# Kernel optimization log

Hardware: AMD Instinct MI355X
Metric: run time of the kernel (lower is better)

Reference implementation:

```python
import jax, jax.numpy as jnp
import numpy as np


def setup_inputs() -> dict:
    key = jax.random.key(0)
    k1, k2 = jax.random.split(key)
    B, EMB, CODES, NUM_TOKENS = 16, 64, 16384, 1024
    x_in = jax.random.normal(k1, (B, EMB, CODES), dtype=jnp.float32)
    code_embedding = jax.random.uniform(k2, (NUM_TOKENS, EMB), dtype=jnp.float32)
    return {"x_in": x_in, "code_embedding": code_embedding}


def reference(x_in, code_embedding):
    # x_in: [B, emb, codes]; code_embedding: [num_tokens, emb]
    x_t = jnp.transpose(x_in, (0, 2, 1))  # [B, codes, emb]
    # squared euclidean distances (argmin is invariant to sqrt used by cdist)
    x2 = jnp.sum(x_t * x_t, axis=-1)                      # [B, codes]
    e2 = jnp.sum(code_embedding * code_embedding, axis=-1)  # [num_tokens]
    dots = jnp.einsum('bce,ke->bck', x_t, code_embedding)   # [B, codes, num_tokens]
    dist2 = x2[:, :, None] - 2.0 * dots + e2[None, None, :]
    indices = jnp.argmin(dist2, axis=2)                   # [B, codes]
    x_out = jnp.transpose(code_embedding[indices], (0, 2, 1))  # [B, emb, codes]
    return x_out, indices[:, :, None]  # indices keepdim like torch argmin(keepdim=True)
```

## Files before the change

kernel.cpp:

```cpp
#include <hip/hip_runtime.h>


#define BB 16
#define EMB 64
#define CODES 16384
#define NT 1024
#define NTILES 64
#define CHUNK 8
#define EPOCHS (NTILES / CHUNK)
#define QPB 256

typedef __attribute__((ext_vector_type(8))) short s16x8;
typedef __attribute__((ext_vector_type(4))) float f32x4;
typedef __attribute__((ext_vector_type(4))) int i32x4;
typedef unsigned int u32;

__device__ inline short bf16_hi(float f) { return (short)(__builtin_bit_cast(u32, f) >> 16); }
__device__ inline float hi_part(float f) { return __builtin_bit_cast(float, __builtin_bit_cast(u32, f) & 0xFFFF0000u); }
__device__ inline u32 umax_(u32 a, u32 b) { return a > b ? a : b; }

__device__ inline void async_copy16(const char* g, char* lds_base_uniform) {
  __builtin_amdgcn_global_load_lds(
      (const __attribute__((address_space(1))) unsigned int*)g,
      (__attribute__((address_space(3))) unsigned int*)(unsigned int)(unsigned long long)lds_base_uniform,
      16, 0, 0);
}

#define WSE_OFF   0
#define WSH_OFF   266240
#define WSH2_OFF  270336

__global__ __launch_bounds__(256) void vq_prep(const float* __restrict__ E,
                                               char* __restrict__ wsE,
                                               float* __restrict__ wsh,
                                               float* __restrict__ wsh2) {
  const int bid = blockIdx.x, tid = threadIdx.x;
  if (bid < 32) {
    const int gid = bid * 256 + tid;
    const int nt = gid >> 7, ks = (gid >> 6) & 1, lane = gid & 63;
    const int col = lane & 15, quad = lane >> 4;
    const int n = nt * 16 + col;
    const int k0 = ks * 32 + quad * 8;
    const float* ep = E + n * EMB + k0;
    s16x8 hv, lv;
    #pragma unroll
    for (int j = 0; j < 8; ++j) {
      float v = ep[j];
      float hf = hi_part(v);
      hv[j] = bf16_hi(v);
      lv[j] = bf16_hi(v - hf);
    }
    char* base = wsE + ((size_t)nt << 12) + ((size_t)ks << 10) + lane * 16;
    *(i32x4*)(base)        = __builtin_bit_cast(i32x4, hv);
    *(i32x4*)(base + 2048) = __builtin_bit_cast(i32x4, lv);
  } else {
    const int n = (bid - 32) * 256 + tid;
    if (n < NT) {
      const float4* ep = (const float4*)(E + n * EMB);
      float s = 0.f;
      #pragma unroll
      for (int g = 0; g < 16; ++g) { float4 v = ep[g]; s += v.x*v.x + v.y*v.y + v.z*v.z + v.w*v.w; }
      const float h = -0.5f * s;
      wsh[n] = h;
      wsh2[n] = 16384.f * (h + 128.f);
    }
  }
}

__global__ __launch_bounds__(512, 4) void vq_main(
    const float* __restrict__ x, const float* __restrict__ E,
    const char* __restrict__ wsE, const float* __restrict__ wsh,
    const float* __restrict__ wsh2,
    float* __restrict__ xout, float* __restrict__ iout) {
  __shared__ char smem[2 * CHUNK * 4096 + 4096];
  float* lh = (float*)(smem + 2 * CHUNK * 4096);
  const int tid = threadIdx.x;
  const int wave = tid >> 6, lane = tid & 63;
  const int col = lane & 15, quad = lane >> 4;
  const int b = blockIdx.y;
  const int c0 = blockIdx.x * QPB;
  const int cw = c0 + wave * 32;

  ((float2*)lh)[tid] = ((const float2*)wsh2)[tid];
  {
    const char* g = wsE + wave * 4096 + lane * 16;
    char* lb = smem + wave * 4096;
    async_copy16(g,        lb);
    async_copy16(g + 1024, lb + 1024);
    async_copy16(g + 2048, lb + 2048);
    async_copy16(g + 3072, lb + 3072);
  }

  s16x8 ah[2][2], al[2][2];
  #pragma unroll
  for (int mt = 0; mt < 2; ++mt) {
    #pragma unroll
    for (int ks = 0; ks < 2; ++ks) {
      s16x8 hv, lv;
      #pragma unroll
      for (int j = 0; j < 8; ++j) {
        const int e = ks * 32 + quad * 8 + j;
        float v = x[((size_t)b * EMB + e) * CODES + (size_t)(cw + mt * 16 + col)] * 16384.f;
        float hf = hi_part(v);
        hv[j] = bf16_hi(v);
        lv[j] = bf16_hi(v - hf);
      }
      ah[mt][ks] = hv;
      al[mt][ks] = lv;
    }
  }

  u32 k1[2][4], k2[2][4];
  #pragma unroll
  for (int mt = 0; mt < 2; ++mt)
    #pragma unroll
    for (int r = 0; r < 4; ++r) { k1[mt][r] = 0u; k2[mt][r] = 0u; }

  u32 inv = 1023u - (u32)col;

  __syncthreads();

  for (int c = 0; c < EPOCHS; ++c) {
    if (c < EPOCHS - 1) {
      const char* g = wsE + (size_t)(c + 1) * (CHUNK * 4096) + wave * 4096 + lane * 16;
      char* lb = smem + ((c + 1) & 1) * (CHUNK * 4096) + wave * 4096;
      async_copy16(g,        lb);
      async_copy16(g + 1024, lb + 1024);
      async_copy16(g + 2048, lb + 2048);
      async_copy16(g + 3072, lb + 3072);
    }

    const char* rb = smem + (c & 1) * (CHUNK * 4096) + lane * 16;
    i32x4 fb0 = *(const i32x4*)(rb);
    i32x4 fb1 = *(const i32x4*)(rb + 1024);
    i32x4 fb2 = *(const i32x4*)(rb + 2048);
    i32x4 fb3 = *(const i32x4*)(rb + 3072);
    float ch = lh[(c * CHUNK) * 16 + col];

    #pragma unroll
    for (int t = 0; t < CHUNK; ++t) {
      i32x4 nb0, nb1, nb2, nb3; float nch;
      if (t < CHUNK - 1) {
        const char* p = rb + (t + 1) * 4096;
        nb0 = *(const i32x4*)(p);
        nb1 = *(const i32x4*)(p + 1024);
        nb2 = *(const i32x4*)(p + 2048);
        nb3 = *(const i32x4*)(p + 3072);
        nch = lh[(c * CHUNK + t + 1) * 16 + col];
      }
      const s16x8 bh0 = __builtin_bit_cast(s16x8, fb0);
      const s16x8 bh1 = __builtin_bit_cast(s16x8, fb1);
      const s16x8 bl0 = __builtin_bit_cast(s16x8, fb2);
      const s16x8 bl1 = __builtin_bit_cast(s16x8, fb3);
      const f32x4 cq = (f32x4){ch, ch, ch, ch};
      const f32x4 zz = (f32x4){0.f, 0.f, 0.f, 0.f};

      #pragma unroll
      for (int mt = 0; mt < 2; ++mt) {
        f32x4 cA = __builtin_amdgcn_mfma_f32_16x16x32_bf16(ah[mt][0], bh0, cq, 0, 0, 0);
        f32x4 cB = __builtin_amdgcn_mfma_f32_16x16x32_bf16(al[mt][1], bh1, zz, 0, 0, 0);
        cA = __builtin_amdgcn_mfma_f32_16x16x32_bf16(ah[mt][1], bh1, cA, 0, 0, 0);
        cB = __builtin_amdgcn_mfma_f32_16x16x32_bf16(ah[mt][0], bl0, cB, 0, 0, 0);
        cA = __builtin_amdgcn_mfma_f32_16x16x32_bf16(al[mt][0], bh0, cA, 0, 0, 0);
        cB = __builtin_amdgcn_mfma_f32_16x16x32_bf16(ah[mt][1], bl1, cB, 0, 0, 0);
        const f32x4 a = cA + cB;

        #pragma unroll
        for (int r = 0; r < 4; ++r) {
          u32 q = (u32)a[r];
          u32 key = (q << 10) + inv;
          u32 k1o = k1[mt][r];
          asm("v_med3_u32 %0, %1, %2, %3"
              : "=v"(k2[mt][r]) : "v"(key), "v"(k1o), "v"(k2[mt][r]));
          k1[mt][r] = umax_(key, k1o);
        }
      }
      inv -= 16u;
      if (t < CHUNK - 1) { fb0 = nb0; fb1 = nb1; fb2 = nb2; fb3 = nb3; ch = nch; }
    }
    __syncthreads();
  }

  uint2* cand = (uint2*)smem;
  int* idxs = (int*)(smem + 2048);
  #pragma unroll
  for (int mt = 0; mt < 2; ++mt) {
    #pragma unroll
    for (int r = 0; r < 4; ++r) {
      u32 a1 = k1[mt][r], a2 = k2[mt][r];
      #pragma unroll
      for (int m = 1; m <= 8; m <<= 1) {
        u32 r1 = __shfl_xor(a1, m, 64);
        u32 r2 = __shfl_xor(a2, m, 64);
        u32 t = a1 < r1 ? a1 : r1;
        a1 = umax_(a1, r1);
        a2 = umax_(umax_(a2, r2), t);
      }
      if (col == r) cand[wave * 32 + mt * 16 + quad * 4 + r] = make_uint2(a1, a2);
    }
  }
  __syncthreads();

  {
    const int q = tid >> 1, which = tid & 1;
    const u32 K = which ? cand[q].y : cand[q].x;
    const int i = 1023 - (int)(K & 1023u);
    const float* xq = x + (size_t)b * EMB * CODES + (size_t)(c0 + q);
    const float4* ei = (const float4*)(E + i * EMB);
    float d0 = 0, d1 = 0, d2 = 0, d3 = 0;
    #pragma unroll
    for (int g = 0; g < 16; ++g) {
      float4 a = ei[g];
      d0 = fmaf(xq[(size_t)(4 * g + 0) * CODES], a.x, d0);
      d1 = fmaf(xq[(size_t)(4 * g + 1) * CODES], a.y, d1);
      d2 = fmaf(xq[(size_t)(4 * g + 2) * CODES], a.z, d2);
      d3 = fmaf(xq[(size_t)(4 * g + 3) * CODES], a.w, d3);
    }
    const float s = ((d0 + d1) + (d2 + d3)) + wsh[i];
    const float s_o = __shfl_xor(s, 1, 64);
    const int i_o = __shfl_xor(i, 1, 64);
    if (which == 0) {
      const bool take2 = (s_o > s) || (s_o == s && i_o < i);
      const int idx = take2 ? i_o : i;
      idxs[q] = idx;
      iout[(size_t)b * CODES + (size_t)(c0 + q)] = (float)idx;
    }
  }
  __syncthreads();

  {
    const int q = tid & (QPB - 1);
    const int eh = (tid >> 8) * 32;
    const int idx = idxs[q];
    const float* Er = E + idx * EMB + eh;
    float* xo = xout + ((size_t)b * EMB + eh) * CODES + (size_t)(c0 + q);
    #pragma unroll
    for (int e = 0; e < 32; ++e) xo[(size_t)e * CODES] = Er[e];
  }
}

extern "C" void kernel_launch(void* const* d_in, const int* in_sizes, int n_in,
                              void* d_out, int out_size, void* d_ws, size_t ws_size,
                              hipStream_t stream) {
  const float* x = (const float*)d_in[0];
  const float* E = (const float*)d_in[1];
  float* xout = (float*)d_out;
  float* iout = (float*)d_out + (size_t)BB * EMB * CODES;

  char* wsE  = (char*)d_ws + WSE_OFF;
  float* wsh  = (float*)((char*)d_ws + WSH_OFF);
  float* wsh2 = (float*)((char*)d_ws + WSH2_OFF);

  vq_prep<<<36, 256, 0, stream>>>(E, wsE, wsh, wsh2);
  vq_main<<<dim3(CODES / QPB, BB), 512, 0, stream>>>(x, E, wsE, wsh, wsh2, xout, iout);
}
```

Before: 208.5 us.

## Software-pipeline tile loop with inline-asm LDS reads and deferred top-2 update

Replaces the per-tile unrolled loop with hand-scheduled inline-asm ds_read_b128 loads that double-buffer tiles in registers, gated by explicit lgkmcnt waits and sched barriers. The MFMAs for both row tiles are interleaved into independent chains. The argmin top-2 key update for each tile is deferred until the next tile's MFMAs are issued, and a final update runs after the loop. The goal is to hide LDS latency and the MFMA dependency chains behind independent work. In exchange it adds register pressure from the extra live accumulators and takes scheduling control away from the compiler.

```diff
diff --git a/kernel.cpp b/kernel.cpp
--- a/kernel.cpp
+++ b/kernel.cpp
@@ -67,6 +67,64 @@
   }
 }
 
+#define DS_READ_TILE(d0, d1, d2, d3, base, T)                               \
+  asm volatile("ds_read_b128 %0, %4 offset:%c5\n\t"                         \
+               "ds_read_b128 %1, %4 offset:%c6\n\t"                         \
+               "ds_read_b128 %2, %4 offset:%c7\n\t"                         \
+               "ds_read_b128 %3, %4 offset:%c8"                             \
+               : "=v"(d0), "=v"(d1), "=v"(d2), "=v"(d3)                     \
+               : "v"(base), "i"((T) * 4096), "i"((T) * 4096 + 1024),        \
+                 "i"((T) * 4096 + 2048), "i"((T) * 4096 + 3072))
+
+#define WAIT_SB(N)                                                          \
+  do {                                                                      \
+    asm volatile("s_waitcnt lgkmcnt(" #N ")");                              \
+    __builtin_amdgcn_sched_barrier(0);                                      \
+  } while (0)
+
+#define MFMA16 __builtin_amdgcn_mfma_f32_16x16x32_bf16
+
+#define TILE_MATH(F0, F1, F2, F3, CH)                                       \
+  do {                                                                      \
+    const s16x8 bh0 = __builtin_bit_cast(s16x8, F0);                        \
+    const s16x8 bh1 = __builtin_bit_cast(s16x8, F1);                        \
+    const s16x8 bl0 = __builtin_bit_cast(s16x8, F2);                        \
+    const s16x8 bl1 = __builtin_bit_cast(s16x8, F3);                        \
+    const f32x4 cq = (f32x4){CH, CH, CH, CH};                               \
+    const f32x4 zz = (f32x4){0.f, 0.f, 0.f, 0.f};                           \
+    f32x4 cA0 = MFMA16(ah[0][0], bh0, cq, 0, 0, 0);                         \
+    f32x4 cB0 = MFMA16(al[0][1], bh1, zz, 0, 0, 0);                         \
+    f32x4 cA1 = MFMA16(ah[1][0], bh0, cq, 0, 0, 0);                         \
+    f32x4 cB1 = MFMA16(al[1][1], bh1, zz, 0, 0, 0);                         \
+    cA0 = MFMA16(ah[0][1], bh1, cA0, 0, 0, 0);                              \
+    cB0 = MFMA16(ah[0][0], bl0, cB0, 0, 0, 0);                              \
+    cA1 = MFMA16(ah[1][1], bh1, cA1, 0, 0, 0);                              \
+    cB1 = MFMA16(ah[1][0], bl0, cB1, 0, 0, 0);                              \
+    cA0 = MFMA16(al[0][0], bh0, cA0, 0, 0, 0);                              \
+    cB0 = MFMA16(ah[0][1], bl1, cB0, 0, 0, 0);                              \
+    cA1 = MFMA16(al[1][0], bh0, cA1, 0, 0, 0);                              \
+    cB1 = MFMA16(ah[1][1], bl1, cB1, 0, 0, 0);                              \
+    TOP2(aPrev0, 0);                                                        \
+    TOP2(aPrev1, 1);                                                        \
+    aPrev0 = cA0 + cB0;                                                     \
+    aPrev1 = cA1 + cB1;                                                     \
+    invPrev = invCur;                                                       \
+    invCur -= 16u;                                                          \
+  } while (0)
+
+#define TOP2(AV, MT)                                                        \
+  do {                                                                      \
+    _Pragma("unroll")                                                       \
+    for (int r = 0; r < 4; ++r) {                                           \
+      u32 q = (u32)AV[r];                        \
+      u32 key = (q << 10) + invPrev;                                        \
+      u32 k1o = k1[MT][r];                                                  \
+      asm("v_med3_u32 %0, %1, %2, %3"                                       \
+          : "=v"(k2[MT][r]) : "v"(key), "v"(k1o), "v"(k2[MT][r]));          \
+      k1[MT][r] = umax_(key, k1o);                                          \
+    }                                                                       \
+  } while (0)
+
 __global__ __launch_bounds__(512, 4) void vq_main(
     const float* __restrict__ x, const float* __restrict__ E,
     const char* __restrict__ wsE, const float* __restrict__ wsh,
@@ -116,7 +174,10 @@
     #pragma unroll
     for (int r = 0; r < 4; ++r) { k1[mt][r] = 0u; k2[mt][r] = 0u; }
 
-  u32 inv = 1023u - (u32)col;
+  f32x4 aPrev0 = (f32x4){0.f, 0.f, 0.f, 0.f};
+  f32x4 aPrev1 = (f32x4){0.f, 0.f, 0.f, 0.f};
+  u32 invCur = 1023u - (u32)col;
+  u32 invPrev = 0u;
 
   __syncthreads();
 
@@ -130,56 +191,60 @@
       async_copy16(g + 3072, lb + 3072);
     }
 
-    const char* rb = smem + (c & 1) * (CHUNK * 4096) + lane * 16;
-    i32x4 fb0 = *(const i32x4*)(rb);
-    i32x4 fb1 = *(const i32x4*)(rb + 1024);
-    i32x4 fb2 = *(const i32x4*)(rb + 2048);
-    i32x4 fb3 = *(const i32x4*)(rb + 3072);
-    float ch = lh[(c * CHUNK) * 16 + col];
-
-    #pragma unroll
-    for (int t = 0; t < CHUNK; ++t) {
-      i32x4 nb0, nb1, nb2, nb3; float nch;
-      if (t < CHUNK - 1) {
-        const char* p = rb + (t + 1) * 4096;
-        nb0 = *(const i32x4*)(p);
-        nb1 = *(const i32x4*)(p + 1024);
-        nb2 = *(const i32x4*)(p + 2048);
-        nb3 = *(const i32x4*)(p + 3072);
-        nch = lh[(c * CHUNK + t + 1) * 16 + col];
-      }
-      const s16x8 bh0 = __builtin_bit_cast(s16x8, fb0);
-      const s16x8 bh1 = __builtin_bit_cast(s16x8, fb1);
-      const s16x8 bl0 = __builtin_bit_cast(s16x8, fb2);
-      const s16x8 bl1 = __builtin_bit_cast(s16x8, fb3);
-      const f32x4 cq = (f32x4){ch, ch, ch, ch};
-      const f32x4 zz = (f32x4){0.f, 0.f, 0.f, 0.f};
-
-      #pragma unroll
-      for (int mt = 0; mt < 2; ++mt) {
-        f32x4 cA = __builtin_amdgcn_mfma_f32_16x16x32_bf16(ah[mt][0], bh0, cq, 0, 0, 0);
-        f32x4 cB = __builtin_amdgcn_mfma_f32_16x16x32_bf16(al[mt][1], bh1, zz, 0, 0, 0);
-        cA = __builtin_amdgcn_mfma_f32_16x16x32_bf16(ah[mt][1], bh1, cA, 0, 0, 0);
-        cB = __builtin_amdgcn_mfma_f32_16x16x32_bf16(ah[mt][0], bl0, cB, 0, 0, 0);
-        cA = __builtin_amdgcn_mfma_f32_16x16x32_bf16(al[mt][0], bh0, cA, 0, 0, 0);
-        cB = __builtin_amdgcn_mfma_f32_16x16x32_bf16(ah[mt][1], bl1, cB, 0, 0, 0);
-        const f32x4 a = cA + cB;
-
-        #pragma unroll
-        for (int r = 0; r < 4; ++r) {
-          u32 q = (u32)a[r];
-          u32 key = (q << 10) + inv;
-          u32 k1o = k1[mt][r];
-          asm("v_med3_u32 %0, %1, %2, %3"
-              : "=v"(k2[mt][r]) : "v"(key), "v"(k1o), "v"(k2[mt][r]));
-          k1[mt][r] = umax_(key, k1o);
-        }
-      }
-      inv -= 16u;
-      if (t < CHUNK - 1) { fb0 = nb0; fb1 = nb1; fb2 = nb2; fb3 = nb3; ch = nch; }
-    }
+    const float ch0 = lh[(c * CHUNK + 0) * 16 + col];
+    const float ch1 = lh[(c * CHUNK + 1) * 16 + col];
+    const float ch2 = lh[(c * CHUNK + 2) * 16 + col];
+    const float ch3 = lh[(c * CHUNK + 3) * 16 + col];
+    const float ch4 = lh[(c * CHUNK + 4) * 16 + col];
+    const float ch5 = lh[(c * CHUNK + 5) * 16 + col];
+    const float ch6 = lh[(c * CHUNK + 6) * 16 + col];
+    const float ch7 = lh[(c * CHUNK + 7) * 16 + col];
+    asm volatile("" :: "v"(ch0), "v"(ch1), "v"(ch2), "v"(ch3),
+                       "v"(ch4), "v"(ch5), "v"(ch6), "v"(ch7));
+
+    const unsigned base =
+        (unsigned)(unsigned long long)(smem) +
+        (unsigned)((c & 1) * (CHUNK * 4096)) + (unsigned)(lane * 16);
+
+    i32x4 tA0, tA1, tA2, tA3, tB0, tB1, tB2, tB3;
+    DS_READ_TILE(tA0, tA1, tA2, tA3, base, 0);
+
+    DS_READ_TILE(tB0, tB1, tB2, tB3, base, 1);
+    WAIT_SB(4);
+    TILE_MATH(tA0, tA1, tA2, tA3, ch0);
+
+    DS_READ_TILE(tA0, tA1, tA2, tA3, base, 2);
+    WAIT_SB(4);
+    TILE_MATH(tB0, tB1, tB2, tB3, ch1);
+
+    DS_READ_TILE(tB0, tB1, tB2, tB3, base, 3);
+    WAIT_SB(4);
+    TILE_MATH(tA0, tA1, tA2, tA3, ch2);
+
+    DS_READ_TILE(tA0, tA1, tA2, tA3, base, 4);
+    WAIT_SB(4);
+    TILE_MATH(tB0, tB1, tB2, tB3, ch3);
+
+    DS_READ_TILE(tB0, tB1, tB2, tB3, base, 5);
+    WAIT_SB(4);
+    TILE_MATH(tA0, tA1, tA2, tA3, ch4);
+
+    DS_READ_TILE(tA0, tA1, tA2, tA3, base, 6);
+    WAIT_SB(4);
+    TILE_MATH(tB0, tB1, tB2, tB3, ch5);
+
+    DS_READ_TILE(tB0, tB1, tB2, tB3, base, 7);
+    WAIT_SB(4);
+    TILE_MATH(tA0, tA1, tA2, tA3, ch6);
+
+    WAIT_SB(0);
+    TILE_MATH(tB0, tB1, tB2, tB3, ch7);
+
     __syncthreads();
   }
+
+  TOP2(aPrev0, 0);
+  TOP2(aPrev1, 1);
 
   uint2* cand = (uint2*)smem;
   int* idxs = (int*)(smem + 2048);
```

Measured after the change: 207.1 us. No clear change (-0.6%).
